# Optimization experiments

Measured on AMD Instinct MI355X. Metric: run time of the kernel, lower is better.

## Reference

```python
import jax, jax.numpy as jnp
import numpy as np

EMBED_DIM = 512
NUM_HEADS = 8
HEAD_DIM = EMBED_DIM // NUM_HEADS
SCALING = HEAD_DIM ** -0.5
T, B = 2048, 4
NEG_INF = -1e9


def setup_inputs() -> dict:
    key = jax.random.key(0)
    k1, k2, k3 = jax.random.split(key, 3)
    h = jax.random.normal(k1, (T, B, EMBED_DIM), dtype=jnp.float32)
    # causal additive mask, [T, T]: 0 on/below diagonal, -inf above
    attn_mask = jnp.where(jnp.triu(jnp.ones((T, T), dtype=bool), k=1), NEG_INF, 0.0).astype(jnp.float32)
    in_proj_weight = jax.random.normal(k2, (3 * EMBED_DIM, EMBED_DIM), dtype=jnp.float32) * 0.02
    in_proj_bias = jnp.zeros((3 * EMBED_DIM,), dtype=jnp.float32)
    out_w = jax.random.normal(k3, (EMBED_DIM, EMBED_DIM), dtype=jnp.float32) * 0.02
    out_b = jnp.zeros((EMBED_DIM,), dtype=jnp.float32)
    return {"h": h, "attn_mask": attn_mask, "in_proj_weight": in_proj_weight,
            "in_proj_bias": in_proj_bias, "out_w": out_w, "out_b": out_b}


def reference(h, attn_mask, in_proj_weight, in_proj_bias, out_w, out_b):
    tgt_len, bsz, embed_dim = h.shape
    # fused QKV projection: [T, B, 3E]
    qkv = jnp.einsum('tbe,fe->tbf', h, in_proj_weight) + in_proj_bias
    q, k, v = jnp.split(qkv, 3, axis=-1)
    q = q * SCALING
    # [T, B, E] -> [B*H, T, hd]
    def to_heads(x):
        return x.reshape(tgt_len, bsz * NUM_HEADS, HEAD_DIM).transpose(1, 0, 2)
    q, k, v = to_heads(q), to_heads(k), to_heads(v)
    # scores: [B*H, T, S]
    attn_weights = jnp.einsum('bth,bsh->bts', q, k)
    attn_weights = attn_weights + attn_mask[None, :, :]
    attn_p = jax.nn.softmax(attn_weights, axis=-1)
    attn = jnp.einsum('bts,bsh->bth', attn_p, v)
    # [B*H, T, hd] -> [T, B, E]
    attn = attn.transpose(1, 0, 2).reshape(tgt_len, bsz, embed_dim)
    out = jnp.einsum('tbe,fe->tbf', attn, out_w) + out_b
    return out, attn_p.reshape(bsz, NUM_HEADS, tgt_len, tgt_len)
```

## Files before the change

### kernel.cpp

```cpp
#include <hip/hip_runtime.h>
#include <cstdint>
#include <cstddef>

#define T_SEQ 2048
#define BSZ 4
#define EMB 512
#define NH 8
#define HD 64
#define SCALING 0.125f
#define NEGBIG (-1e30f)
#define PW 144

typedef short bf16x8_t __attribute__((ext_vector_type(8)));
typedef float f32x4_t __attribute__((ext_vector_type(4)));
typedef short short4v __attribute__((ext_vector_type(4)));
typedef float float4v __attribute__((ext_vector_type(4)));

typedef __attribute__((address_space(1))) const void* as1_cvp;
typedef __attribute__((address_space(3))) void* as3_vp;

#define MFMA16(a, b, c) __builtin_amdgcn_mfma_f32_16x16x32_bf16((a), (b), (c), 0, 0, 0)

static __device__ __forceinline__ short f2b(float f) {
  union { float f; uint32_t u; } x; x.f = f;
  uint32_t r = (x.u + 0x7fffu + ((x.u >> 16) & 1u)) >> 16;
  return (short)(r & 0xffffu);
}

static __device__ __forceinline__ void gload_lds16(const void* g, void* l) {
  __builtin_amdgcn_global_load_lds((as1_cvp)g, (as3_vp)l, 16, 0, 0);
}

__global__ __launch_bounds__(256)
void cvt3_kernel(const float* __restrict__ a, const float* __restrict__ b,
                 const float* __restrict__ c, short* __restrict__ oa,
                 short* __restrict__ ob, short* __restrict__ oc) {
  const int bid = blockIdx.x;
  const float* in;
  short* out;
  int base;
  if (bid < 4096)      { in = a; out = oa; base = bid; }
  else if (bid < 4864) { in = b; out = ob; base = bid - 4096; }
  else                 { in = c; out = oc; base = bid - 4864; }
  int i = (base * 256 + threadIdx.x) * 4;
  float4v v = *(const float4v*)(in + i);
  short4v o;
  o[0] = f2b(v[0]); o[1] = f2b(v[1]); o[2] = f2b(v[2]); o[3] = f2b(v[3]);
  *(short4v*)(out + i) = o;
}

template <int EPI>
__global__ __launch_bounds__(256)
void gemm_bt(const short* __restrict__ A, const short* __restrict__ Bt,
             const float* __restrict__ bias,
             short* __restrict__ outQ, short* __restrict__ outK, short* __restrict__ outV,
             float* __restrict__ outF) {
  __shared__ short ldsA[128 * 32];
  __shared__ short ldsB[128 * 32];
  const int tid = threadIdx.x;
  const int wid = tid >> 6, lane = tid & 63, g = lane >> 4, r16 = lane & 15;
  const int wr = wid >> 1, wc = wid & 1;
  const int mbase = blockIdx.y * 128, nbase = blockIdx.x * 128;

  f32x4_t acc[4][4];
#pragma unroll
  for (int m = 0; m < 4; ++m)
#pragma unroll
    for (int n = 0; n < 4; ++n) acc[m][n] = (f32x4_t){0.f, 0.f, 0.f, 0.f};

  for (int kt = 0; kt < 16; ++kt) {
    __syncthreads();
#pragma unroll
    for (int i = 0; i < 2; ++i) {
      int c = i * 256 + tid;
      int row = c >> 2, j4 = c & 3;
      gload_lds16(A + (size_t)(mbase + row) * 512 + kt * 32 + j4 * 8, &ldsA[c * 8]);
      gload_lds16(Bt + (size_t)(nbase + row) * 512 + kt * 32 + j4 * 8, &ldsB[c * 8]);
    }
    __syncthreads();
    bf16x8_t af[4], bfv[4];
#pragma unroll
    for (int m = 0; m < 4; ++m)
      af[m] = *(const bf16x8_t*)&ldsA[(wr * 64 + m * 16 + r16) * 32 + g * 8];
#pragma unroll
    for (int n = 0; n < 4; ++n)
      bfv[n] = *(const bf16x8_t*)&ldsB[(wc * 64 + n * 16 + r16) * 32 + g * 8];
#pragma unroll
    for (int m = 0; m < 4; ++m)
#pragma unroll
      for (int n = 0; n < 4; ++n) acc[m][n] = MFMA16(af[m], bfv[n], acc[m][n]);
  }

#pragma unroll
  for (int m = 0; m < 4; ++m) {
#pragma unroll
    for (int n = 0; n < 4; ++n) {
      int col = nbase + wc * 64 + n * 16 + r16;
      float bcol = bias[col];
#pragma unroll
      for (int j = 0; j < 4; ++j) {
        int row = mbase + wr * 64 + m * 16 + g * 4 + j;
        float v = acc[m][n][j] + bcol;
        if (EPI == 0) {
          int sect = col >> 9, e = col & 511, hh = e >> 6, d = e & 63;
          int t = row >> 2, b = row & 3;
          size_t dst = ((size_t)(b * NH + hh) * T_SEQ + t) * HD + d;
          short bv = f2b(v);
          if (sect == 0) outQ[dst] = bv;
          else if (sect == 1) outK[dst] = bv;
          else outV[dst] = bv;
        } else {
          outF[(size_t)row * EMB + col] = v;
        }
      }
    }
  }
}

__global__ __launch_bounds__(256)
void attn_fused(const short* __restrict__ Qg, const short* __restrict__ Kg,
                const short* __restrict__ Vg, float* __restrict__ Pout,
                short* __restrict__ attnO) {
  __shared__ __align__(16) short lds[26624];
  short* Kt = lds;
  short* Vt = lds + 8192;
  short(*Pl)[16 * PW] = (short(*)[16 * PW])(lds + 8192 + 9216);
  const int fid = (int)(blockIdx.y * gridDim.x + blockIdx.x);
  const int xcd = fid & 7, slot = fid >> 3;
  const int bh = (xcd << 2) | (slot & 3);
  const int qt = 31 - (slot >> 2);
  const int tid = threadIdx.x, wid = tid >> 6, lane = tid & 63;
  const int g = lane >> 4, r16 = lane & 15;
  const size_t headOff = (size_t)bh * T_SEQ * HD;
  const int wrow0 = qt * 64 + wid * 16;
  const int myrow = wrow0 + r16;
  const int maxcol = qt * 64 + 64;
  const int nt128 = (qt >> 1) + 1;
  const short* Kh = Kg + headOff;
  const short* Vh = Vg + headOff;

  bf16x8_t qf[2];
  {
    const short* qp = Qg + headOff + (size_t)myrow * HD + g * 8;
    qf[0] = *(const bf16x8_t*)qp;
    qf[1] = *(const bf16x8_t*)(qp + 32);
  }

  float m_w = NEGBIG;
  float l_w = 0.f;
  f32x4_t oacc[4];
#pragma unroll
  for (int dc = 0; dc < 4; ++dc) oacc[dc] = (f32x4_t){0.f, 0.f, 0.f, 0.f};

  uint32_t* Vtu = (uint32_t*)Vt;
  const int kp0 = tid & 63, dg0 = tid >> 6;

  bf16x8_t va[2], vb[2];
#define VLOAD(KB)                                                              \
  {                                                                            \
    const short* vp0 = Vh + (size_t)((KB) + kp0 * 2) * HD + dg0 * 8;           \
    va[0] = *(const bf16x8_t*)vp0; vb[0] = *(const bf16x8_t*)(vp0 + HD);       \
    const short* vp1 = vp0 + 32;                                               \
    va[1] = *(const bf16x8_t*)vp1; vb[1] = *(const bf16x8_t*)(vp1 + HD);       \
  }
  VLOAD(0)

  for (int kt = 0; kt < nt128; ++kt) {
    const int kb = kt * 128;
    __syncthreads();
#pragma unroll
    for (int i = 0; i < 4; ++i) {
      int cc = i * 256 + tid;
      int row = cc >> 3, j8 = (cc & 7) ^ (row & 7);
      gload_lds16(Kh + (size_t)(kb + row) * HD + j8 * 8, &Kt[cc * 8]);
    }
#pragma unroll
    for (int i = 0; i < 2; ++i) {
      int dg = dg0 + i * 4;
#pragma unroll
      for (int j = 0; j < 8; ++j)
        Vtu[(dg * 8 + j) * (PW / 2) + kp0] =
            (uint32_t)(uint16_t)va[i][j] | ((uint32_t)(uint16_t)vb[i][j] << 16);
    }
    __syncthreads();
    if (kt + 1 < nt128) VLOAD(kb + 128)
    const int H = ((maxcol - kb) >= 128) ? 2 : 1;
#pragma unroll
    for (int h = 0; h < 2; ++h) {
      if (h < H) {
        float sv[4][4];
#pragma unroll
        for (int kc4 = 0; kc4 < 4; ++kc4) {
          const int rl = (h * 4 + kc4) * 16 + r16;
          f32x4_t s = {0.f, 0.f, 0.f, 0.f};
#pragma unroll
          for (int kk = 0; kk < 2; ++kk) {
            int byteo = (rl * 128 + kk * 64 + g * 16) ^ ((rl & 7) << 4);
            bf16x8_t kf = *(const bf16x8_t*)((const char*)Kt + byteo);
            s = MFMA16(kf, qf[kk], s);
          }
          const int key0 = kb + (h * 4 + kc4) * 16 + g * 4;
#pragma unroll
          for (int j = 0; j < 4; ++j)
            sv[kc4][j] = (key0 + j <= myrow) ? s[j] * SCALING : NEGBIG;
        }
        float pm = NEGBIG;
#pragma unroll
        for (int kc4 = 0; kc4 < 4; ++kc4)
#pragma unroll
          for (int j = 0; j < 4; ++j) pm = fmaxf(pm, sv[kc4][j]);
#pragma unroll
        for (int off = 1; off < 64; off <<= 1) pm = fmaxf(pm, __shfl_xor(pm, off));
        float mn = fmaxf(m_w, pm);
        if (mn > m_w + 8.f) {
          float sc = __expf(m_w - mn);
          l_w *= sc;
#pragma unroll
          for (int dc = 0; dc < 4; ++dc)
#pragma unroll
            for (int j = 0; j < 4; ++j) oacc[dc][j] *= sc;
          m_w = mn;
        }
#pragma unroll
        for (int kc4 = 0; kc4 < 4; ++kc4) {
          short4v pb;
#pragma unroll
          for (int j = 0; j < 4; ++j) {
            float e = __expf(sv[kc4][j] - m_w);
            l_w += e;
            pb[j] = f2b(e);
          }
          *(short4v*)&Pl[wid][r16 * PW + (h * 4 + kc4) * 16 + g * 4] = pb;
        }
#pragma unroll
        for (int kk2 = 0; kk2 < 2; ++kk2) {
          const int kc2 = h * 2 + kk2;
          bf16x8_t pf = *(const bf16x8_t*)&Pl[wid][r16 * PW + kc2 * 32 + g * 8];
#pragma unroll
          for (int dc = 0; dc < 4; ++dc) {
            bf16x8_t vf = *(const bf16x8_t*)&Vt[(dc * 16 + r16) * PW + kc2 * 32 + g * 8];
            oacc[dc] = MFMA16(pf, vf, oacc[dc]);
          }
        }
      }
    }
  }

#pragma unroll
  for (int off = 16; off <= 32; off <<= 1) l_w += __shfl_xor(l_w, off);
  const float rl2 = 1.0f / l_w;

  float lo[4];
#pragma unroll
  for (int j = 0; j < 4; ++j) lo[j] = 1.0f / __shfl(l_w, g * 4 + j);
#pragma unroll
  for (int dc = 0; dc < 4; ++dc) {
#pragma unroll
    for (int j = 0; j < 4; ++j) {
      int t = wrow0 + g * 4 + j, d = dc * 16 + r16;
      size_t ntok = (size_t)t * BSZ + (bh >> 3);
      attnO[ntok * EMB + (bh & 7) * HD + d] = f2b(oacc[dc][j] * lo[j]);
    }
  }

  short* Kb0 = lds;
  short* Kb1 = lds + 8192;
  float* Prow = Pout + ((size_t)bh * T_SEQ + myrow) * T_SEQ;

#define STAGEK(KB, BUF)                                                        \
  {                                                                            \
    _Pragma("unroll")                                                          \
    for (int i = 0; i < 4; ++i) {                                              \
      int cc = i * 256 + tid;                                                  \
      int row = cc >> 3, j8 = (cc & 7) ^ (row & 7);                            \
      gload_lds16(Kh + (size_t)((KB) + row) * HD + j8 * 8, &(BUF)[cc * 8]);    \
    }                                                                          \
  }

  __syncthreads();
  STAGEK(0, Kb0)
  __syncthreads();
  int p = 0;
  for (int kt = 0; kt < nt128; ++kt) {
    const int kb = kt * 128;
    short* cur = p ? Kb1 : Kb0;
    short* nxt = p ? Kb0 : Kb1;
    const bool more = (kt + 1 < nt128);
    if (more) {
      STAGEK(kb + 128, nxt)
      __builtin_amdgcn_sched_barrier(0);
    }
    const int navail = (maxcol - kb) >> 4;
    const int nkc = navail < 8 ? navail : 8;
#pragma unroll
    for (int kc = 0; kc < 8; ++kc) {
      if (kc < nkc) {
        const int rl = kc * 16 + r16;
        f32x4_t s = {0.f, 0.f, 0.f, 0.f};
#pragma unroll
        for (int kk = 0; kk < 2; ++kk) {
          int byteo = (rl * 128 + kk * 64 + g * 16) ^ ((rl & 7) << 4);
          bf16x8_t kf = *(const bf16x8_t*)((const char*)cur + byteo);
          s = MFMA16(kf, qf[kk], s);
        }
        const int key0 = kb + kc * 16 + g * 4;
        float4v pvv;
#pragma unroll
        for (int j = 0; j < 4; ++j) {
          float e = __expf(s[j] * SCALING - m_w) * rl2;
          pvv[j] = (key0 + j <= myrow) ? e : 0.f;
        }
        *(float4v*)(Prow + key0) = pvv;
      }
    }
    if (more) {
      __builtin_amdgcn_sched_barrier(0);
      asm volatile("s_waitcnt vmcnt(8)" ::: "memory");
      __builtin_amdgcn_s_barrier();
      __builtin_amdgcn_sched_barrier(0);
    }
    p ^= 1;
  }

  const int c0 = maxcol;
  const int nc4 = (T_SEQ - c0) >> 2;
  for (int r = 0; r < 64; ++r) {
    size_t base = ((size_t)bh * T_SEQ + qt * 64 + r) * T_SEQ + c0;
    for (int c4 = tid; c4 < nc4; c4 += 256) {
      float4v z = {0.f, 0.f, 0.f, 0.f};
      *(float4v*)(Pout + base + (size_t)c4 * 4) = z;
    }
  }
}

extern "C" void kernel_launch(void* const* d_in, const int* in_sizes, int n_in,
                              void* d_out, int out_size, void* d_ws, size_t ws_size,
                              hipStream_t stream) {
  const float* h = (const float*)d_in[0];
  const float* w_in = (const float*)d_in[2];
  const float* b_in = (const float*)d_in[3];
  const float* w_out = (const float*)d_in[4];
  const float* b_out = (const float*)d_in[5];
  float* out = (float*)d_out;
  float* Pout = out + (size_t)T_SEQ * BSZ * EMB;

  short* hB = (short*)d_ws;
  short* wB = hB + (size_t)8192 * 512;
  short* owB = wB + (size_t)1536 * 512;
  short* qB = owB + (size_t)512 * 512;
  short* kB = qB + (size_t)32 * 2048 * 64;
  short* vB = kB + (size_t)32 * 2048 * 64;
  short* aB = vB + (size_t)32 * 2048 * 64;

  cvt3_kernel<<<5120, 256, 0, stream>>>(h, w_in, w_out, hB, wB, owB);

  gemm_bt<0><<<dim3(12, 64), 256, 0, stream>>>(hB, wB, b_in, qB, kB, vB, nullptr);
  attn_fused<<<dim3(32, 32), 256, 0, stream>>>(qB, kB, vB, Pout, aB);
  gemm_bt<1><<<dim3(4, 64), 256, 0, stream>>>(aB, owB, b_out, nullptr, nullptr, nullptr, out);
}
```

Baseline: 221.2 us.

## Double-buffer GEMM LDS tiles and stage probability rows through LDS for coalesced stores

The projection GEMM now double-buffers its A/B LDS tiles, prefetching the next k-slice while MFMAs run on the current one, instead of two full barriers per iteration. In the attention-probability pass, each wave writes its 16x64 block of probabilities into a padded LDS scratch (odd stride 67). It then reads the block back row-wise so each row segment goes to global memory as contiguous float4 stores rather than scattered column-strided writes. This targets the cost of the large fp32 probability output and the load latency in the GEMM. In exchange it uses more LDS, which may lower occupancy, and processes keys in 64-wide halves instead of 16-wide chunks.

```diff
diff --git a/kernel.cpp b/kernel.cpp
--- a/kernel.cpp
+++ b/kernel.cpp
@@ -10,6 +10,7 @@
 #define SCALING 0.125f
 #define NEGBIG (-1e30f)
 #define PW 144
+#define PSW 67
 
 typedef short bf16x8_t __attribute__((ext_vector_type(8)));
 typedef float f32x4_t __attribute__((ext_vector_type(4)));
@@ -55,8 +56,8 @@
              const float* __restrict__ bias,
              short* __restrict__ outQ, short* __restrict__ outK, short* __restrict__ outV,
              float* __restrict__ outF) {
-  __shared__ short ldsA[128 * 32];
-  __shared__ short ldsB[128 * 32];
+  __shared__ short ldsA[2][128 * 32];
+  __shared__ short ldsB[2][128 * 32];
   const int tid = threadIdx.x;
   const int wid = tid >> 6, lane = tid & 63, g = lane >> 4, r16 = lane & 15;
   const int wr = wid >> 1, wc = wid & 1;
@@ -68,27 +69,48 @@
 #pragma unroll
     for (int n = 0; n < 4; ++n) acc[m][n] = (f32x4_t){0.f, 0.f, 0.f, 0.f};
 
+#define GSTAGE(KT, PP)                                                         \
+  {                                                                            \
+    _Pragma("unroll")                                                          \
+    for (int i = 0; i < 2; ++i) {                                              \
+      int c = i * 256 + tid;                                                   \
+      int row = c >> 2, j4 = c & 3;                                            \
+      gload_lds16(A + (size_t)(mbase + row) * 512 + (KT) * 32 + j4 * 8,        \
+                  &ldsA[PP][c * 8]);                                           \
+      gload_lds16(Bt + (size_t)(nbase + row) * 512 + (KT) * 32 + j4 * 8,       \
+                  &ldsB[PP][c * 8]);                                           \
+    }                                                                          \
+  }
+
+  GSTAGE(0, 0)
+  asm volatile("s_waitcnt vmcnt(0)" ::: "memory");
+  __builtin_amdgcn_s_barrier();
+  __builtin_amdgcn_sched_barrier(0);
+  int p = 0;
   for (int kt = 0; kt < 16; ++kt) {
-    __syncthreads();
-#pragma unroll
-    for (int i = 0; i < 2; ++i) {
-      int c = i * 256 + tid;
-      int row = c >> 2, j4 = c & 3;
-      gload_lds16(A + (size_t)(mbase + row) * 512 + kt * 32 + j4 * 8, &ldsA[c * 8]);
-      gload_lds16(Bt + (size_t)(nbase + row) * 512 + kt * 32 + j4 * 8, &ldsB[c * 8]);
-    }
-    __syncthreads();
+    const bool more = (kt + 1 < 16);
+    if (more) {
+      GSTAGE(kt + 1, p ^ 1)
+      __builtin_amdgcn_sched_barrier(0);
+    }
     bf16x8_t af[4], bfv[4];
 #pragma unroll
     for (int m = 0; m < 4; ++m)
-      af[m] = *(const bf16x8_t*)&ldsA[(wr * 64 + m * 16 + r16) * 32 + g * 8];
+      af[m] = *(const bf16x8_t*)&ldsA[p][(wr * 64 + m * 16 + r16) * 32 + g * 8];
 #pragma unroll
     for (int n = 0; n < 4; ++n)
-      bfv[n] = *(const bf16x8_t*)&ldsB[(wc * 64 + n * 16 + r16) * 32 + g * 8];
+      bfv[n] = *(const bf16x8_t*)&ldsB[p][(wc * 64 + n * 16 + r16) * 32 + g * 8];
 #pragma unroll
     for (int m = 0; m < 4; ++m)
 #pragma unroll
       for (int n = 0; n < 4; ++n) acc[m][n] = MFMA16(af[m], bfv[n], acc[m][n]);
+    if (more) {
+      __builtin_amdgcn_sched_barrier(0);
+      asm volatile("s_waitcnt vmcnt(0)" ::: "memory");
+      __builtin_amdgcn_s_barrier();
+      __builtin_amdgcn_sched_barrier(0);
+      p ^= 1;
+    }
   }
 
 #pragma unroll
@@ -265,7 +287,8 @@
 
   short* Kb0 = lds;
   short* Kb1 = lds + 8192;
-  float* Prow = Pout + ((size_t)bh * T_SEQ + myrow) * T_SEQ;
+  float* Pst = (float*)(lds + 8192 + 9216);
+  float* Pstw = Pst + wid * 16 * PSW;
 
 #define STAGEK(KB, BUF)                                                        \
   {                                                                            \
@@ -291,26 +314,38 @@
       __builtin_amdgcn_sched_barrier(0);
     }
     const int navail = (maxcol - kb) >> 4;
-    const int nkc = navail < 8 ? navail : 8;
-#pragma unroll
-    for (int kc = 0; kc < 8; ++kc) {
-      if (kc < nkc) {
-        const int rl = kc * 16 + r16;
-        f32x4_t s = {0.f, 0.f, 0.f, 0.f};
-#pragma unroll
-        for (int kk = 0; kk < 2; ++kk) {
-          int byteo = (rl * 128 + kk * 64 + g * 16) ^ ((rl & 7) << 4);
-          bf16x8_t kf = *(const bf16x8_t*)((const char*)cur + byteo);
-          s = MFMA16(kf, qf[kk], s);
-        }
-        const int key0 = kb + kc * 16 + g * 4;
-        float4v pvv;
-#pragma unroll
-        for (int j = 0; j < 4; ++j) {
-          float e = __expf(s[j] * SCALING - m_w) * rl2;
-          pvv[j] = (key0 + j <= myrow) ? e : 0.f;
-        }
-        *(float4v*)(Prow + key0) = pvv;
+    const int H2 = (navail >= 8) ? 2 : 1;
+#pragma unroll
+    for (int h = 0; h < 2; ++h) {
+      if (h < H2) {
+#pragma unroll
+        for (int kc4 = 0; kc4 < 4; ++kc4) {
+          const int kc = h * 4 + kc4;
+          const int rl = kc * 16 + r16;
+          f32x4_t s = {0.f, 0.f, 0.f, 0.f};
+#pragma unroll
+          for (int kk = 0; kk < 2; ++kk) {
+            int byteo = (rl * 128 + kk * 64 + g * 16) ^ ((rl & 7) << 4);
+            bf16x8_t kf = *(const bf16x8_t*)((const char*)cur + byteo);
+            s = MFMA16(kf, qf[kk], s);
+          }
+          const int key0 = kb + kc * 16 + g * 4;
+          float4v pvv;
+#pragma unroll
+          for (int j = 0; j < 4; ++j) {
+            float e = __expf(s[j] * SCALING - m_w) * rl2;
+            pvv[j] = (key0 + j <= myrow) ? e : 0.f;
+          }
+          *(float4v*)&Pstw[r16 * PSW + kc4 * 16 + g * 4] = pvv;
+        }
+#pragma unroll
+        for (int i = 0; i < 4; ++i) {
+          int row = i * 4 + (lane >> 4);
+          int c16 = lane & 15;
+          float4v t = *(const float4v*)&Pstw[row * PSW + c16 * 4];
+          *(float4v*)(Pout + ((size_t)bh * T_SEQ + wrow0 + row) * T_SEQ +
+                      kb + h * 64 + c16 * 4) = t;
+        }
       }
     }
     if (more) {
```

New measurement: 235.4 us. 6.4% more time.
